# Kernel tuning notes

Hardware: AMD Instinct MI355X
Metric: run time of the kernel (lower is better)

The kernel has to match this reference:

```python
import jax, jax.numpy as jnp
import numpy as np
import math

Q_DIM = 1024
K_DIM = 1024
ATT_DIM = 1024
POS_DIM = 64
B, NQ, NK = 4, 2048, 2048
EPS = 1e-5


def _ln(x, g, b):
    m = jnp.mean(x, axis=-1, keepdims=True)
    v = jnp.var(x, axis=-1, keepdims=True)
    return (x - m) * jax.lax.rsqrt(v + EPS) * g + b


def _sinpos(n, dim):
    # SinPos: exp = 2*arange(dim//2)/dim; pos = p * 10000**-exp; cat(pos, pos+pi/2); sin
    e = 2.0 * jnp.arange(dim // 2, dtype=jnp.float32) / dim      # [dim/2]
    p = jnp.arange(n, dtype=jnp.float32)[:, None]                # [n,1]
    ph = p * jnp.power(10000.0, -e)[None, :]                     # [n,dim/2]
    return jnp.sin(jnp.concatenate([ph, ph + math.pi / 2], axis=1))  # [n,dim]


def setup_inputs() -> dict:
    key = jax.random.key(0)
    ks = jax.random.split(key, 8)
    s = 0.02
    return {
        "q": jax.random.normal(ks[0], (B, NQ, Q_DIM), jnp.float32),
        "k": jax.random.normal(ks[1], (B, NK, K_DIM), jnp.float32),
        "Wq": jax.random.normal(ks[2], (Q_DIM, ATT_DIM), jnp.float32) * s,
        "bq": jnp.zeros((ATT_DIM,), jnp.float32),
        "Wk": jax.random.normal(ks[3], (K_DIM, ATT_DIM), jnp.float32) * s,
        "bk": jnp.zeros((ATT_DIM,), jnp.float32),
        "Wv": jax.random.normal(ks[4], (K_DIM, ATT_DIM), jnp.float32) * s,
        "bv": jnp.zeros((ATT_DIM,), jnp.float32),
        "gq": jnp.ones((ATT_DIM,), jnp.float32), "betaq": jnp.zeros((ATT_DIM,), jnp.float32),
        "gk": jnp.ones((ATT_DIM,), jnp.float32), "betak": jnp.zeros((ATT_DIM,), jnp.float32),
        "gv": jnp.ones((ATT_DIM,), jnp.float32), "betav": jnp.zeros((ATT_DIM,), jnp.float32),
        "Wp": jax.random.normal(ks[5], (POS_DIM, POS_DIM), jnp.float32) * s,
        "bp": jnp.zeros((POS_DIM,), jnp.float32),
    }


def reference(q, k, Wq, bq, Wk, bk, Wv, bv, gq, betaq, gk, betak, gv, betav, Wp, bp):
    qn = _ln(q @ Wq + bq, gq, betaq)          # [B,NQ,D]
    vn = _ln(k @ Wv + bv, gv, betav)          # [B,NK,D]
    kn = _ln(k @ Wk + bk, gk, betak)          # [B,NK,D]
    pos = _sinpos(NK, POS_DIM)                # [NK,P]

    # attention 1: Q=qn, K=kn, V=pos
    s1 = jnp.einsum('bnd,bjd->bnj', qn, kn) * (1.0 / math.sqrt(ATT_DIM))
    a1 = jax.nn.softmax(s1, axis=-1)          # [B,NQ,NK]
    x = jnp.einsum('bnj,jp->bnp', a1, pos)    # [B,NQ,P]

    # pos_net (Linear)
    x = x @ Wp + bp                           # [B,NQ,P]

    # attention 2: Q=x, K=pos, V=vn
    s2 = jnp.einsum('bnp,jp->bnj', x, pos) * (1.0 / math.sqrt(POS_DIM))
    a2 = jax.nn.softmax(s2, axis=-1)          # [B,NQ,NK]
    out = jnp.einsum('bnj,bjd->bnd', a2, vn)  # [B,NQ,D]

    att = jnp.stack([a1, a2], axis=1)         # [B,2,NQ,NK] == torch.cat over head dim
    return out, att
```

## Files before the change

### kernel.cpp

```cpp
#include <hip/hip_runtime.h>
#include <math.h>
#include <stdint.h>


typedef _Float16 f16;
typedef _Float16 f16x4 __attribute__((ext_vector_type(4)));
typedef _Float16 f16x8 __attribute__((ext_vector_type(8)));
typedef float f32x4 __attribute__((ext_vector_type(4)));

static constexpr int CB  = 4;
static constexpr int CNQ = 2048;
static constexpr int CNK = 2048;
static constexpr int CD  = 1024;
static constexpr int CP  = 64;

static __device__ __forceinline__ void async16(const f16* gp, f16* lp) {
  __builtin_amdgcn_global_load_lds(
      (const __attribute__((address_space(1))) void*)(uintptr_t)gp,
      (__attribute__((address_space(3))) void*)(uint32_t)(uintptr_t)lp,
      16, 0, 0);
}

__global__ __launch_bounds__(256) void pos_kernel(f16* __restrict__ posb,
                                                  f16* __restrict__ posTb) {
  int tid = blockIdx.x * 256 + threadIdx.x;
  int p = tid >> 11;
  int j = tid & (CNK - 1);
  int i = p & 31;
  float ph = (float)j * powf(10000.0f, -(float)i * (1.0f / 32.0f));
  float v = (p < 32) ? sinf(ph) : cosf(ph);
  posb[j * CP + p]   = (f16)v;
  posTb[p * CNK + j] = (f16)v;
}

__global__ __launch_bounds__(256) void cvt2_kernel(const float* __restrict__ a,
                                                   const float* __restrict__ b,
                                                   f16* __restrict__ oa,
                                                   f16* __restrict__ ob) {
  const int NF4 = CB * CNQ * CD / 4;
  int tid = blockIdx.x * 256 + threadIdx.x;
  const float* src = (tid < NF4) ? a : b;
  f16* dst = (tid < NF4) ? oa : ob;
  int i = (tid < NF4) ? tid : tid - NF4;
  float4 v = reinterpret_cast<const float4*>(src)[i];
  f16x4 o = {(f16)v.x, (f16)v.y, (f16)v.z, (f16)v.w};
  reinterpret_cast<f16x4*>(dst)[i] = o;
}

__global__ __launch_bounds__(256) void cvtWT_kernel(
    const float* __restrict__ Wq, const float* __restrict__ Wk,
    const float* __restrict__ Wv, f16* __restrict__ WqT, f16* __restrict__ WkvT) {
  __shared__ float t[64][65];
  const float* W = (blockIdx.z == 0) ? Wq : (blockIdx.z == 1) ? Wk : Wv;
  f16* WT = (blockIdx.z == 0) ? WqT : (blockIdx.z == 1) ? WkvT : WkvT + 1024 * 1024;
  int k0 = blockIdx.x * 64, n0 = blockIdx.y * 64;
  int tx = threadIdx.x & 63, ty = threadIdx.x >> 6;
#pragma unroll
  for (int i = 0; i < 16; i++)
    t[ty + 4 * i][tx] = W[(size_t)(k0 + ty + 4 * i) * CD + n0 + tx];
  __syncthreads();
#pragma unroll
  for (int i = 0; i < 16; i++)
    WT[(size_t)(n0 + 4 * i + ty) * CD + k0 + tx] = (f16)t[tx][ty + 4 * i];
}

__global__ __launch_bounds__(256) void transpose_kernel(const f16* __restrict__ in,
                                                        f16* __restrict__ out,
                                                        int ldi) {
  __shared__ f16 t[64][65];
  int n0 = blockIdx.x * 64, d0 = blockIdx.y * 64;
  size_t ibase = (size_t)blockIdx.z * CNK * ldi;
  size_t obase = (size_t)blockIdx.z * CNK * CD;
  int tx = threadIdx.x & 63, ty = threadIdx.x >> 6;
#pragma unroll
  for (int i = 0; i < 16; i++)
    t[ty + 4 * i][tx] = in[ibase + (size_t)(n0 + ty + 4 * i) * ldi + d0 + tx];
  __syncthreads();
#pragma unroll
  for (int i = 0; i < 16; i++)
    out[obase + (size_t)(d0 + ty + 4 * i) * CNK + n0 + tx] = t[tx][ty + 4 * i];
}

template <int BM, int BN>
__device__ __forceinline__ void gemm_core(
    const f16* __restrict__ Ab, const f16* __restrict__ Bb,
    int lda, int ldb, int K, int m0, int n0, f16* sm,
    f32x4 (&acc)[BM / 32][BN / 64]) {
  constexpr int FM = BM / 32, FN = BN / 64;
  constexpr int TI = (BM + BN) / 64;
  constexpr int bufsz = (BM + BN) * 64;
  const int tid = threadIdx.x;
  const int lane = tid & 63, wid = tid >> 6;
  const int wr = wid >> 2, wc = wid & 3;
  const int lrow = lane & 15, kg = lane >> 4;

  auto stage = [&](int i, int kt, int buf) {
    const int s = i * 512 + tid;
    const int row = s >> 3;
    const int cb = (s & 7) << 4;
    const int scb = cb ^ ((row & 7) << 4);
    const f16* src = (i < BM / 64)
        ? Ab + (size_t)(m0 + row) * lda + kt * 64 + (scb >> 1)
        : Bb + (size_t)(n0 + row - BM) * ldb + kt * 64 + (scb >> 1);
    async16(src, &sm[buf * bufsz + s * 8]);
  };

  const int NT = K >> 6;
#pragma unroll
  for (int i = 0; i < TI; i++) stage(i, 0, 0);

  for (int t = 0; t < NT; ++t) {
    const int cur = t & 1;
    if (t + 1 < NT) {
#pragma unroll
      for (int i = 0; i < TI; i++) stage(i, t + 1, cur ^ 1);
      if constexpr (TI == 8) asm volatile("s_waitcnt vmcnt(8)" ::: "memory");
      else                   asm volatile("s_waitcnt vmcnt(6)" ::: "memory");
    } else {
      asm volatile("s_waitcnt vmcnt(0)" ::: "memory");
    }
    __builtin_amdgcn_s_barrier();

    const f16* smA = sm + cur * bufsz;
    const f16* smB = smA + BM * 64;
#pragma unroll
    for (int kk = 0; kk < 2; ++kk) {
      const int Cb = kk * 64 + kg * 16;
      f16x8 af[FM], bf[FN];
#pragma unroll
      for (int m = 0; m < FM; ++m) {
        const int ar = wr * (BM / 2) + m * 16 + lrow;
        af[m] = *reinterpret_cast<const f16x8*>(
            &smA[ar * 64 + ((Cb ^ ((ar & 7) << 4)) >> 1)]);
      }
#pragma unroll
      for (int n = 0; n < FN; ++n) {
        const int br = wc * (BN / 4) + n * 16 + lrow;
        bf[n] = *reinterpret_cast<const f16x8*>(
            &smB[br * 64 + ((Cb ^ ((br & 7) << 4)) >> 1)]);
      }
      __builtin_amdgcn_s_barrier();
      __builtin_amdgcn_s_setprio(1);
#pragma unroll
      for (int m = 0; m < FM; ++m)
#pragma unroll
        for (int n = 0; n < FN; ++n)
          acc[m][n] = __builtin_amdgcn_mfma_f32_16x16x32_f16(af[m], bf[n], acc[m][n], 0, 0, 0);
      __builtin_amdgcn_s_setprio(0);
      __builtin_amdgcn_s_barrier();
    }
  }
}

template <int BM, int BN>
__device__ __forceinline__ void epi_f16(
    f32x4 (&acc)[BM / 32][BN / 64], f16* sm, f16* Cp, int ldc, int m0, int n0) {
  const int tid = threadIdx.x, lane = tid & 63, wid = tid >> 6;
  const int wr = wid >> 2, wc = wid & 3;
  const int rbase = wr * (BM / 2) + (lane >> 4) * 4;
  const int cbase = wc * (BN / 4) + (lane & 15);
  __syncthreads();
#pragma unroll
  for (int mg = 0; mg < BM / 32; mg++)
#pragma unroll
    for (int n = 0; n < BN / 64; n++)
#pragma unroll
      for (int r = 0; r < 4; r++)
        sm[(rbase + mg * 16 + r) * BN + cbase + n * 16] = (f16)acc[mg][n][r];
  __syncthreads();
  constexpr int CH = BM * BN / (512 * 8);
#pragma unroll
  for (int c = 0; c < CH; c++) {
    const int idx = c * 512 + tid;
    const int row = idx / (BN / 8);
    const int cole = (idx % (BN / 8)) * 8;
    f16x8 v = *reinterpret_cast<const f16x8*>(&sm[row * BN + cole]);
    *reinterpret_cast<f16x8*>(Cp + (size_t)(m0 + row) * ldc + n0 + cole) = v;
  }
}

template <int BM, int BN>
__device__ __forceinline__ void epi_exp(
    f32x4 (&acc)[BM / 32][BN / 64], f16* sm, float* psum, f16* Cp, int ldc,
    int m0, int n0, float scale, float* PSrow) {
  const int tid = threadIdx.x, lane = tid & 63, wid = tid >> 6;
  const int wr = wid >> 2, wc = wid & 3;
  const int rbase = wr * (BM / 2) + (lane >> 4) * 4;
  const int cbase = wc * (BN / 4) + (lane & 15);
  __syncthreads();
  if (tid < BM) psum[tid] = 0.f;
#pragma unroll
  for (int mg = 0; mg < BM / 32; mg++)
#pragma unroll
    for (int n = 0; n < BN / 64; n++)
#pragma unroll
      for (int r = 0; r < 4; r++)
        sm[(rbase + mg * 16 + r) * BN + cbase + n * 16] =
            (f16)__expf(acc[mg][n][r] * scale);
  __syncthreads();
  constexpr int CH = BM * BN / (512 * 8);
#pragma unroll
  for (int c = 0; c < CH; c++) {
    const int idx = c * 512 + tid;
    const int row = idx / (BN / 8);
    const int cole = (idx % (BN / 8)) * 8;
    f16x8 v = *reinterpret_cast<const f16x8*>(&sm[row * BN + cole]);
    *reinterpret_cast<f16x8*>(Cp + (size_t)(m0 + row) * ldc + n0 + cole) = v;
    float p = 0.f;
#pragma unroll
    for (int j = 0; j < 8; j++) p += (float)v[j];
#pragma unroll
    for (int o = 1; o < 32; o <<= 1) p += __shfl_xor(p, o);
    if ((lane & 31) == 0) atomicAdd(&psum[row], p);
  }
  __syncthreads();
  if (tid < BM) PSrow[tid] = psum[tid];
}

template <int BM, int BN>
__device__ __forceinline__ void epi_f32(
    f32x4 (&acc)[BM / 32][BN / 64], f16* smh, float* Cp, int ldc, int m0, int n0) {
  float* st = (float*)smh;
  const int tid = threadIdx.x, lane = tid & 63, wid = tid >> 6;
  const int wr = wid >> 2, wc = wid & 3;
  const int cbase = wc * (BN / 4) + (lane & 15);
#pragma unroll
  for (int half = 0; half < 2; half++) {
    __syncthreads();
    if (wr == half) {
#pragma unroll
      for (int mg = 0; mg < BM / 32; mg++)
#pragma unroll
        for (int r = 0; r < 4; r++) {
          const int rloc = (lane >> 4) * 4 + mg * 16 + r;
#pragma unroll
          for (int n = 0; n < BN / 64; n++)
            st[rloc * BN + cbase + n * 16] = acc[mg][n][r];
        }
    }
    __syncthreads();
    constexpr int CH = (BM / 2) * BN / (512 * 4);
#pragma unroll
    for (int c = 0; c < CH; c++) {
      const int idx = c * 512 + tid;
      const int row = idx / (BN / 4);
      const int cole = (idx % (BN / 4)) * 4;
      float4 v = *reinterpret_cast<const float4*>(&st[row * BN + cole]);
      *reinterpret_cast<float4*>(
          Cp + (size_t)(m0 + half * (BM / 2) + row) * ldc + n0 + cole) = v;
    }
  }
}

__global__ __launch_bounds__(512) void gemmIn_kernel(
    const f16* __restrict__ q16, const f16* __restrict__ WqT, f16* __restrict__ tmpq,
    const f16* __restrict__ k16, const f16* __restrict__ WkvT, f16* __restrict__ tmp2) {
  __shared__ __attribute__((aligned(16))) f16 sm[2][(256 + 128) * 64];
  const int b = blockIdx.x;
  const int swz = (b & 7) * 96 + (b >> 3);
  const f16 *A, *B;
  f16* C;
  int ldc, m0, n0;
  if (swz < 256) {
    const int by = swz >> 5, bx = swz & 31;
    A = q16; B = WqT; C = tmpq; ldc = 1024; m0 = bx * 256; n0 = by * 128;
  } else {
    const int idx = swz - 256;
    const int by = idx >> 5, bx = idx & 31;
    A = k16; B = WkvT; C = tmp2; ldc = 2048; m0 = bx * 256; n0 = by * 128;
  }
  f32x4 acc[8][2] = {};
  gemm_core<256, 128>(A, B, 1024, 1024, 1024, m0, n0, &sm[0][0], acc);
  epi_f16<256, 128>(acc, &sm[0][0], C, ldc, m0, n0);
}

__global__ __launch_bounds__(512) void gemmS1_kernel(
    const f16* __restrict__ qn, const f16* __restrict__ kn,
    f16* __restrict__ e1, float* __restrict__ PS) {
  __shared__ __attribute__((aligned(16))) f16 sm[2][(256 + 256) * 64];
  __shared__ float psum[256];
  const int b = blockIdx.x;
  const int swz = (b & 7) * 32 + (b >> 3);
  const int bz = swz >> 6;
  const int rem = swz & 63;
  const int by = rem >> 3, bx = rem & 7;
  const int m0 = bx * 256, n0 = by * 256;
  const f16* Ab = qn + (size_t)bz * 2048 * 1024;
  const f16* Bb = kn + (size_t)bz * 2048 * 2048;
  f16* Cp = e1 + (size_t)bz * 2048 * 2048;
  f32x4 acc[8][4] = {};
  gemm_core<256, 256>(Ab, Bb, 1024, 2048, 1024, m0, n0, &sm[0][0], acc);
  epi_exp<256, 256>(acc, &sm[0][0], psum, Cp, 2048, m0, n0, 0.03125f,
                    PS + (size_t)by * 8192 + bz * 2048 + m0);
}

__global__ __launch_bounds__(512) void gemmOut_kernel(
    const f16* __restrict__ e2, const f16* __restrict__ vnT, float* __restrict__ out) {
  __shared__ __attribute__((aligned(16))) f16 sm[2][(256 + 128) * 64];
  const int b = blockIdx.x;
  const int swz = (b & 7) * 32 + (b >> 3);
  const int bz = swz >> 6;
  const int rem = swz & 63;
  const int by = rem >> 3, bx = rem & 7;
  const int m0 = bx * 256, n0 = by * 128;
  const f16* Ab = e2 + (size_t)bz * 2048 * 2048;
  const f16* Bb = vnT + (size_t)bz * 1024 * 2048;
  float* Cp = out + (size_t)bz * 2048 * 1024;
  f32x4 acc[8][2] = {};
  gemm_core<256, 128>(Ab, Bb, 2048, 2048, 2048, m0, n0, &sm[0][0], acc);
  epi_f32<256, 128>(acc, &sm[0][0], Cp, 1024, m0, n0);
}

__global__ __launch_bounds__(256) void ln3_kernel(
    f16* __restrict__ tmpq, f16* __restrict__ tmp2,
    const float* __restrict__ bq, const float* __restrict__ gq, const float* __restrict__ beq,
    const float* __restrict__ bk, const float* __restrict__ gk, const float* __restrict__ bek,
    const float* __restrict__ bv, const float* __restrict__ gv, const float* __restrict__ bev) {
  __shared__ float rs_[4], rq_[4];
  const int z = blockIdx.y;
  f16* rp;
  const float *bias, *g, *beta;
  if (z == 0)      { rp = tmpq + (size_t)blockIdx.x * 1024;        bias = bq; g = gq; beta = beq; }
  else if (z == 1) { rp = tmp2 + (size_t)blockIdx.x * 2048;        bias = bk; g = gk; beta = bek; }
  else             { rp = tmp2 + (size_t)blockIdx.x * 2048 + 1024; bias = bv; g = gv; beta = bev; }
  const int t = threadIdx.x;
  f16x4 v = *reinterpret_cast<const f16x4*>(rp + t * 4);
  float y[4], s = 0.f, q = 0.f;
#pragma unroll
  for (int j = 0; j < 4; j++) {
    y[j] = (float)v[j] + bias[t * 4 + j];
    s += y[j]; q += y[j] * y[j];
  }
#pragma unroll
  for (int o = 32; o; o >>= 1) { s += __shfl_xor(s, o); q += __shfl_xor(q, o); }
  if ((t & 63) == 0) { rs_[t >> 6] = s; rq_[t >> 6] = q; }
  __syncthreads();
  s = rs_[0] + rs_[1] + rs_[2] + rs_[3];
  q = rq_[0] + rq_[1] + rq_[2] + rq_[3];
  const float mean = s * (1.0f / CD);
  const float rstd = rsqrtf(q * (1.0f / CD) - mean * mean + 1e-5f);
  f16x4 o;
#pragma unroll
  for (int j = 0; j < 4; j++) {
    int c = t * 4 + j;
    o[j] = (f16)((y[j] - mean) * rstd * g[c] + beta[c]);
  }
  *reinterpret_cast<f16x4*>(rp + t * 4) = o;
}

__global__ __launch_bounds__(256) void norm1_kernel(
    const f16* __restrict__ e1, const float* __restrict__ PS,
    float* __restrict__ inv1, float* __restrict__ att) {
  const int row = blockIdx.x;
  const int b = row >> 11, n = row & (CNQ - 1);
  float s = 0.f;
#pragma unroll
  for (int j = 0; j < 8; j++) s += PS[j * (CB * CNQ) + row];
  const float iv = 1.0f / s;
  if (threadIdx.x == 0) inv1[row] = iv;
  const int t = threadIdx.x;
  float* rp = att + ((size_t)(b << 1) * CNQ + n) * CNK;
  f16x8 v = *reinterpret_cast<const f16x8*>(e1 + (size_t)row * CNK + t * 8);
  float4 w0 = {(float)v[0] * iv, (float)v[1] * iv, (float)v[2] * iv, (float)v[3] * iv};
  float4 w1 = {(float)v[4] * iv, (float)v[5] * iv, (float)v[6] * iv, (float)v[7] * iv};
  reinterpret_cast<float4*>(rp)[t * 2]     = w0;
  reinterpret_cast<float4*>(rp)[t * 2 + 1] = w1;
}

__global__ __launch_bounds__(256) void xgemm_kernel(
    const f16* __restrict__ e1, const f16* __restrict__ posTb, float* __restrict__ xw) {
  constexpr int BM = 64, BN = 64;
  __shared__ __attribute__((aligned(16))) f16 As[BM * 32];
  __shared__ __attribute__((aligned(16))) f16 Bs[BN * 32];
  const int lane = threadIdx.x & 63;
  const int wave = threadIdx.x >> 6;
  const int wr = wave >> 1, wc = wave & 1;
  const int m0 = blockIdx.x * BM;
  const int kbase = blockIdx.z * 1024;
  const int srow = lane >> 2;
  const int scol = (lane & 3) * 8;
  const int lrow = lane & 15;
  const int kg = lane >> 4;
  f32x4 acc[2][2] = {};
  for (int k0 = 0; k0 < 1024; k0 += 32) {
    __syncthreads();
#pragma unroll
    for (int i = wave; i < 8; i += 4) {
      if (i < 4)
        async16(e1 + (size_t)(m0 + i * 16 + srow) * CNK + kbase + k0 + scol, &As[i * 512]);
      else
        async16(posTb + (size_t)((i - 4) * 16 + srow) * CNK + kbase + k0 + scol,
                &Bs[(i - 4) * 512]);
    }
    __syncthreads();
    f16x8 af[2], bfr[2];
#pragma unroll
    for (int m = 0; m < 2; m++)
      af[m] = *reinterpret_cast<const f16x8*>(&As[(wr * 32 + m * 16 + lrow) * 32 + kg * 8]);
#pragma unroll
    for (int n = 0; n < 2; n++)
      bfr[n] = *reinterpret_cast<const f16x8*>(&Bs[(wc * 32 + n * 16 + lrow) * 32 + kg * 8]);
#pragma unroll
    for (int m = 0; m < 2; m++)
#pragma unroll
      for (int n = 0; n < 2; n++)
        acc[m][n] = __builtin_amdgcn_mfma_f32_16x16x32_f16(af[m], bfr[n], acc[m][n], 0, 0, 0);
  }
  float* Cp = xw + (size_t)blockIdx.z * (CB * CNQ) * CP;
  const int crow = m0 + wr * 32 + (lane >> 4) * 4;
  const int ccol = wc * 32 + (lane & 15);
#pragma unroll
  for (int m = 0; m < 2; m++)
#pragma unroll
    for (int n = 0; n < 2; n++)
#pragma unroll
      for (int r = 0; r < 4; r++)
        Cp[(size_t)(crow + m * 16 + r) * CP + ccol + n * 16] = acc[m][n][r];
}

__global__ __launch_bounds__(128) void attn2_kernel(
    const float* __restrict__ xw, const float* __restrict__ Wp,
    const float* __restrict__ bp, const f16* __restrict__ posb,
    const float* __restrict__ inv1, f16* __restrict__ e2,
    float* __restrict__ att) {
  __shared__ __attribute__((aligned(16))) f16 shm[32 * 2048 + 32 * 64];
  __shared__ float rsum[32];
  f16* e2lds = shm;
  f16* xpb = shm + 32 * 2048;
  float* xs = (float*)shm;
  float* Wps = (float*)shm + 32 * 64;
  const int tid = threadIdx.x, l = tid & 63, w = tid >> 6;
  const int r0 = blockIdx.x * 32;
#pragma unroll
  for (int i = 0; i < 16; i++) {
    const int row = w * 16 + i;
    const size_t gi = (size_t)(r0 + row) * CP + l;
    xs[row * 64 + l] = (xw[gi] + xw[(size_t)(CB * CNQ) * CP + gi]) * inv1[r0 + row];
  }
#pragma unroll
  for (int i = w; i < 64; i += 2) Wps[i * 64 + l] = Wp[i * 64 + l];
  const float bpl = bp[l];
  __syncthreads();
  const int rb = w * 16;
#pragma unroll 2
  for (int i = 0; i < 16; i++) {
    float a = bpl;
#pragma unroll 8
    for (int p = 0; p < 64; p++) a = fmaf(xs[(rb + i) * 64 + p], Wps[p * 64 + l], a);
    xpb[(rb + i) * 64 + l] = (f16)a;
  }
  __syncthreads();
  const f16x8 af0 = *reinterpret_cast<const f16x8*>(&xpb[(rb + (l & 15)) * 64 + (l >> 4) * 8]);
  const f16x8 af1 = *reinterpret_cast<const f16x8*>(&xpb[(rb + (l & 15)) * 64 + 32 + (l >> 4) * 8]);
  float rs[4] = {0.f, 0.f, 0.f, 0.f};
  for (int jt = 0; jt < CNK / 64; jt++) {
#pragma unroll
    for (int q4 = 0; q4 < 4; q4++) {
      const int j = jt * 64 + q4 * 16 + (l & 15);
      const f16* pp = posb + (size_t)j * CP + (l >> 4) * 8;
      f16x8 b0 = *reinterpret_cast<const f16x8*>(pp);
      f16x8 b1 = *reinterpret_cast<const f16x8*>(pp + 32);
      f32x4 c = {};
      c = __builtin_amdgcn_mfma_f32_16x16x32_f16(af0, b0, c, 0, 0, 0);
      c = __builtin_amdgcn_mfma_f32_16x16x32_f16(af1, b1, c, 0, 0, 0);
#pragma unroll
      for (int r = 0; r < 4; r++) {
        float ev = __expf(c[r] * 0.125f);
        rs[r] += ev;
        e2lds[(rb + (l >> 4) * 4 + r) * 2048 + j] = (f16)ev;
      }
    }
  }
#pragma unroll
  for (int r = 0; r < 4; r++) {
#pragma unroll
    for (int o = 1; o < 16; o <<= 1) rs[r] += __shfl_xor(rs[r], o);
    if ((l & 15) == 0) rsum[rb + (l >> 4) * 4 + r] = rs[r];
  }
  __syncthreads();
  const int b = r0 >> 11, nloc = r0 & (CNQ - 1);
  float* attb = att + ((size_t)((b << 1) + 1) * CNQ + nloc) * CNK;
  f16* e2b = e2 + (size_t)r0 * CNK;
  for (int row = 0; row < 32; row++) {
    const float iv = 1.0f / rsum[row];
    const f16x8 a0 = *reinterpret_cast<const f16x8*>(&e2lds[row * 2048 + tid * 16]);
    const f16x8 a1 = *reinterpret_cast<const f16x8*>(&e2lds[row * 2048 + tid * 16 + 8]);
    float4 w0 = {(float)a0[0] * iv, (float)a0[1] * iv, (float)a0[2] * iv, (float)a0[3] * iv};
    float4 w1 = {(float)a0[4] * iv, (float)a0[5] * iv, (float)a0[6] * iv, (float)a0[7] * iv};
    float4 w2 = {(float)a1[0] * iv, (float)a1[1] * iv, (float)a1[2] * iv, (float)a1[3] * iv};
    float4 w3 = {(float)a1[4] * iv, (float)a1[5] * iv, (float)a1[6] * iv, (float)a1[7] * iv};
    float* ap = attb + (size_t)row * CNK + tid * 16;
    reinterpret_cast<float4*>(ap)[0] = w0;
    reinterpret_cast<float4*>(ap)[1] = w1;
    reinterpret_cast<float4*>(ap)[2] = w2;
    reinterpret_cast<float4*>(ap)[3] = w3;
    f16x8 h0 = {(f16)w0.x, (f16)w0.y, (f16)w0.z, (f16)w0.w,
                (f16)w1.x, (f16)w1.y, (f16)w1.z, (f16)w1.w};
    f16x8 h1 = {(f16)w2.x, (f16)w2.y, (f16)w2.z, (f16)w2.w,
                (f16)w3.x, (f16)w3.y, (f16)w3.z, (f16)w3.w};
    f16* ep = e2b + (size_t)row * CNK + tid * 16;
    *reinterpret_cast<f16x8*>(ep)     = h0;
    *reinterpret_cast<f16x8*>(ep + 8) = h1;
  }
}

extern "C" void kernel_launch(void* const* d_in, const int* in_sizes, int n_in,
                              void* d_out, int out_size, void* d_ws, size_t ws_size,
                              hipStream_t stream) {
  (void)in_sizes; (void)n_in; (void)out_size; (void)ws_size;
  const float* q    = (const float*)d_in[0];
  const float* k    = (const float*)d_in[1];
  const float* Wq   = (const float*)d_in[2];
  const float* bq   = (const float*)d_in[3];
  const float* Wk   = (const float*)d_in[4];
  const float* bk   = (const float*)d_in[5];
  const float* Wv   = (const float*)d_in[6];
  const float* bv   = (const float*)d_in[7];
  const float* gq   = (const float*)d_in[8];
  const float* betaq= (const float*)d_in[9];
  const float* gk   = (const float*)d_in[10];
  const float* betak= (const float*)d_in[11];
  const float* gv   = (const float*)d_in[12];
  const float* betav= (const float*)d_in[13];
  const float* Wp   = (const float*)d_in[14];
  const float* bp   = (const float*)d_in[15];

  float* out = (float*)d_out;
  float* att = out + (size_t)CB * CNQ * CD;
  char* ws = (char*)d_ws;
  const size_t MB = 1ull << 20;

  f16* q16   = (f16*)(ws);
  f16* k16   = (f16*)(ws + 16 * MB);
  f16* e1    = (f16*)(ws);
  f16* e2    = (f16*)(ws);
  f16* WqT   = (f16*)(ws + 32 * MB);
  f16* WkvT  = (f16*)(ws + 34 * MB);
  f16* posb  = (f16*)(ws + 38 * MB);
  f16* posTb = (f16*)(ws + 38 * MB + 256 * 1024);
  float* xw  = (float*)(ws + 38 * MB + 512 * 1024);
  float* PS  = (float*)(ws + 42 * MB + 512 * 1024);
  float* inv1= (float*)(ws + 42 * MB + 768 * 1024);
  f16* tmpq  = (f16*)(ws + 43 * MB);
  f16* tmp2  = (f16*)(ws + 59 * MB);
  f16* vnT   = (f16*)(ws + 91 * MB);
  f16* qn = tmpq;
  f16* kn = tmp2;
  f16* vn = tmp2 + 1024;

  pos_kernel<<<(CP * CNK) / 256, 256, 0, stream>>>(posb, posTb);
  cvt2_kernel<<<2 * (CB * CNQ * CD / 4) / 256, 256, 0, stream>>>(q, k, q16, k16);
  cvtWT_kernel<<<dim3(16, 16, 3), 256, 0, stream>>>(Wq, Wk, Wv, WqT, WkvT);

  gemmIn_kernel<<<768, 512, 0, stream>>>(q16, WqT, tmpq, k16, WkvT, tmp2);
  ln3_kernel<<<dim3(CB * CNQ, 3), 256, 0, stream>>>(
      tmpq, tmp2, bq, gq, betaq, bk, gk, betak, bv, gv, betav);
  transpose_kernel<<<dim3(CNK / 64, CD / 64, CB), 256, 0, stream>>>(vn, vnT, 2048);

  gemmS1_kernel<<<256, 512, 0, stream>>>(qn, kn, e1, PS);
  norm1_kernel<<<CB * CNQ, 256, 0, stream>>>(e1, PS, inv1, att);

  xgemm_kernel<<<dim3(CB * CNQ / 64, 1, 2), 256, 0, stream>>>(e1, posTb, xw);
  attn2_kernel<<<CB * CNQ / 32, 128, 0, stream>>>(xw, Wp, bp, posb, inv1, e2, att);

  gemmOut_kernel<<<256, 512, 0, stream>>>(e2, vnT, out);
}
```

Baseline: 324.1 us.

## Fuse prep kernels, triple-buffer GEMM core, fold softmax normalization into xgemm

Merges the pos, conversion and weight-transpose kernels into one prep launch. Switches the shared GEMM mainloop to a three-stage LDS pipeline. Shrinks the gemmS1 tile to 256x128 with 512 blocks and writes row partial sums directly instead of through LDS atomics. Removes norm1_kernel by having xgemm write the normalized attention-1 probabilities while it streams e1 tiles, and attn2 recomputes the inverse sums from PS. The aim is fewer launches, one less full pass over e1, and better latency hiding, at the cost of more LDS per block (possibly lower occupancy) and 16-way partial-sum reductions.

```diff
diff --git a/kernel.cpp b/kernel.cpp
--- a/kernel.cpp
+++ b/kernel.cpp
@@ -21,47 +21,49 @@
       16, 0, 0);
 }
 
-__global__ __launch_bounds__(256) void pos_kernel(f16* __restrict__ posb,
-                                                  f16* __restrict__ posTb) {
-  int tid = blockIdx.x * 256 + threadIdx.x;
-  int p = tid >> 11;
-  int j = tid & (CNK - 1);
-  int i = p & 31;
-  float ph = (float)j * powf(10000.0f, -(float)i * (1.0f / 32.0f));
-  float v = (p < 32) ? sinf(ph) : cosf(ph);
-  posb[j * CP + p]   = (f16)v;
-  posTb[p * CNK + j] = (f16)v;
-}
-
-__global__ __launch_bounds__(256) void cvt2_kernel(const float* __restrict__ a,
-                                                   const float* __restrict__ b,
-                                                   f16* __restrict__ oa,
-                                                   f16* __restrict__ ob) {
-  const int NF4 = CB * CNQ * CD / 4;
-  int tid = blockIdx.x * 256 + threadIdx.x;
-  const float* src = (tid < NF4) ? a : b;
-  f16* dst = (tid < NF4) ? oa : ob;
-  int i = (tid < NF4) ? tid : tid - NF4;
-  float4 v = reinterpret_cast<const float4*>(src)[i];
-  f16x4 o = {(f16)v.x, (f16)v.y, (f16)v.z, (f16)v.w};
-  reinterpret_cast<f16x4*>(dst)[i] = o;
-}
-
-__global__ __launch_bounds__(256) void cvtWT_kernel(
+__global__ __launch_bounds__(256) void prep_kernel(
+    const float* __restrict__ q, const float* __restrict__ k,
     const float* __restrict__ Wq, const float* __restrict__ Wk,
-    const float* __restrict__ Wv, f16* __restrict__ WqT, f16* __restrict__ WkvT) {
-  __shared__ float t[64][65];
-  const float* W = (blockIdx.z == 0) ? Wq : (blockIdx.z == 1) ? Wk : Wv;
-  f16* WT = (blockIdx.z == 0) ? WqT : (blockIdx.z == 1) ? WkvT : WkvT + 1024 * 1024;
-  int k0 = blockIdx.x * 64, n0 = blockIdx.y * 64;
-  int tx = threadIdx.x & 63, ty = threadIdx.x >> 6;
-#pragma unroll
-  for (int i = 0; i < 16; i++)
-    t[ty + 4 * i][tx] = W[(size_t)(k0 + ty + 4 * i) * CD + n0 + tx];
-  __syncthreads();
-#pragma unroll
-  for (int i = 0; i < 16; i++)
-    WT[(size_t)(n0 + 4 * i + ty) * CD + k0 + tx] = (f16)t[tx][ty + 4 * i];
+    const float* __restrict__ Wv,
+    f16* __restrict__ q16, f16* __restrict__ k16,
+    f16* __restrict__ WqT, f16* __restrict__ WkvT,
+    f16* __restrict__ posb, f16* __restrict__ posTb) {
+  const int b = blockIdx.x;
+  if (b < 512) {
+    int tid = b * 256 + threadIdx.x;
+    int p = tid >> 11;
+    int j = tid & (CNK - 1);
+    int i = p & 31;
+    float ph = (float)j * powf(10000.0f, -(float)i * (1.0f / 32.0f));
+    float v = (p < 32) ? sinf(ph) : cosf(ph);
+    posb[j * CP + p]   = (f16)v;
+    posTb[p * CNK + j] = (f16)v;
+  } else if (b < 512 + 16384) {
+    const int NF4 = CB * CNQ * CD / 4;
+    int tid = (b - 512) * 256 + threadIdx.x;
+    const float* src = (tid < NF4) ? q : k;
+    f16* dst = (tid < NF4) ? q16 : k16;
+    int i = (tid < NF4) ? tid : tid - NF4;
+    float4 v = reinterpret_cast<const float4*>(src)[i];
+    f16x4 o = {(f16)v.x, (f16)v.y, (f16)v.z, (f16)v.w};
+    reinterpret_cast<f16x4*>(dst)[i] = o;
+  } else {
+    __shared__ float t[64][65];
+    const int idx = b - 16896;
+    const int z = idx >> 8;
+    const int rem = idx & 255;
+    const float* W = (z == 0) ? Wq : (z == 1) ? Wk : Wv;
+    f16* WT = (z == 0) ? WqT : (z == 1) ? WkvT : WkvT + 1024 * 1024;
+    int k0 = (rem & 15) * 64, n0 = (rem >> 4) * 64;
+    int tx = threadIdx.x & 63, ty = threadIdx.x >> 6;
+#pragma unroll
+    for (int i = 0; i < 16; i++)
+      t[ty + 4 * i][tx] = W[(size_t)(k0 + ty + 4 * i) * CD + n0 + tx];
+    __syncthreads();
+#pragma unroll
+    for (int i = 0; i < 16; i++)
+      WT[(size_t)(n0 + 4 * i + ty) * CD + k0 + tx] = (f16)t[tx][ty + 4 * i];
+  }
 }
 
 __global__ __launch_bounds__(256) void transpose_kernel(const f16* __restrict__ in,
@@ -82,7 +84,7 @@
 }
 
 template <int BM, int BN>
-__device__ __forceinline__ void gemm_core(
+__device__ __forceinline__ void gemm_core3(
     const f16* __restrict__ Ab, const f16* __restrict__ Bb,
     int lda, int ldb, int K, int m0, int n0, f16* sm,
     f32x4 (&acc)[BM / 32][BN / 64]) {
@@ -108,20 +110,23 @@
   const int NT = K >> 6;
 #pragma unroll
   for (int i = 0; i < TI; i++) stage(i, 0, 0);
+#pragma unroll
+  for (int i = 0; i < TI; i++) stage(i, 1, 1);
 
   for (int t = 0; t < NT; ++t) {
-    const int cur = t & 1;
-    if (t + 1 < NT) {
-#pragma unroll
-      for (int i = 0; i < TI; i++) stage(i, t + 1, cur ^ 1);
-      if constexpr (TI == 8) asm volatile("s_waitcnt vmcnt(8)" ::: "memory");
-      else                   asm volatile("s_waitcnt vmcnt(6)" ::: "memory");
+    if (t + 2 < NT) {
+      const int b2 = (t + 2) % 3;
+#pragma unroll
+      for (int i = 0; i < TI; i++) stage(i, t + 2, b2);
+      asm volatile("s_waitcnt vmcnt(12)" ::: "memory");
+    } else if (t + 2 == NT) {
+      asm volatile("s_waitcnt vmcnt(6)" ::: "memory");
     } else {
       asm volatile("s_waitcnt vmcnt(0)" ::: "memory");
     }
     __builtin_amdgcn_s_barrier();
 
-    const f16* smA = sm + cur * bufsz;
+    const f16* smA = sm + (t % 3) * bufsz;
     const f16* smB = smA + BM * 64;
 #pragma unroll
     for (int kk = 0; kk < 2; ++kk) {
@@ -183,12 +188,12 @@
 __device__ __forceinline__ void epi_exp(
     f32x4 (&acc)[BM / 32][BN / 64], f16* sm, float* psum, f16* Cp, int ldc,
     int m0, int n0, float scale, float* PSrow) {
+  constexpr int SL = BN / 8;
   const int tid = threadIdx.x, lane = tid & 63, wid = tid >> 6;
   const int wr = wid >> 2, wc = wid & 3;
   const int rbase = wr * (BM / 2) + (lane >> 4) * 4;
   const int cbase = wc * (BN / 4) + (lane & 15);
   __syncthreads();
-  if (tid < BM) psum[tid] = 0.f;
 #pragma unroll
   for (int mg = 0; mg < BM / 32; mg++)
 #pragma unroll
@@ -202,16 +207,16 @@
 #pragma unroll
   for (int c = 0; c < CH; c++) {
     const int idx = c * 512 + tid;
-    const int row = idx / (BN / 8);
-    const int cole = (idx % (BN / 8)) * 8;
+    const int row = idx / SL;
+    const int cole = (idx % SL) * 8;
     f16x8 v = *reinterpret_cast<const f16x8*>(&sm[row * BN + cole]);
     *reinterpret_cast<f16x8*>(Cp + (size_t)(m0 + row) * ldc + n0 + cole) = v;
     float p = 0.f;
 #pragma unroll
     for (int j = 0; j < 8; j++) p += (float)v[j];
 #pragma unroll
-    for (int o = 1; o < 32; o <<= 1) p += __shfl_xor(p, o);
-    if ((lane & 31) == 0) atomicAdd(&psum[row], p);
+    for (int o = 1; o < SL; o <<= 1) p += __shfl_xor(p, o);
+    if ((lane & (SL - 1)) == 0) psum[row] = p;
   }
   __syncthreads();
   if (tid < BM) PSrow[tid] = psum[tid];
@@ -255,7 +260,7 @@
 __global__ __launch_bounds__(512) void gemmIn_kernel(
     const f16* __restrict__ q16, const f16* __restrict__ WqT, f16* __restrict__ tmpq,
     const f16* __restrict__ k16, const f16* __restrict__ WkvT, f16* __restrict__ tmp2) {
-  __shared__ __attribute__((aligned(16))) f16 sm[2][(256 + 128) * 64];
+  __shared__ __attribute__((aligned(16))) f16 sm[3 * (256 + 128) * 64];
   const int b = blockIdx.x;
   const int swz = (b & 7) * 96 + (b >> 3);
   const f16 *A, *B;
@@ -270,33 +275,33 @@
     A = k16; B = WkvT; C = tmp2; ldc = 2048; m0 = bx * 256; n0 = by * 128;
   }
   f32x4 acc[8][2] = {};
-  gemm_core<256, 128>(A, B, 1024, 1024, 1024, m0, n0, &sm[0][0], acc);
-  epi_f16<256, 128>(acc, &sm[0][0], C, ldc, m0, n0);
+  gemm_core3<256, 128>(A, B, 1024, 1024, 1024, m0, n0, sm, acc);
+  epi_f16<256, 128>(acc, sm, C, ldc, m0, n0);
 }
 
 __global__ __launch_bounds__(512) void gemmS1_kernel(
     const f16* __restrict__ qn, const f16* __restrict__ kn,
     f16* __restrict__ e1, float* __restrict__ PS) {
-  __shared__ __attribute__((aligned(16))) f16 sm[2][(256 + 256) * 64];
+  __shared__ __attribute__((aligned(16))) f16 sm[3 * (256 + 128) * 64];
   __shared__ float psum[256];
   const int b = blockIdx.x;
-  const int swz = (b & 7) * 32 + (b >> 3);
-  const int bz = swz >> 6;
-  const int rem = swz & 63;
+  const int swz = (b & 7) * 64 + (b >> 3);
+  const int bz = swz >> 7;
+  const int rem = swz & 127;
   const int by = rem >> 3, bx = rem & 7;
-  const int m0 = bx * 256, n0 = by * 256;
+  const int m0 = bx * 256, n0 = by * 128;
   const f16* Ab = qn + (size_t)bz * 2048 * 1024;
   const f16* Bb = kn + (size_t)bz * 2048 * 2048;
   f16* Cp = e1 + (size_t)bz * 2048 * 2048;
-  f32x4 acc[8][4] = {};
-  gemm_core<256, 256>(Ab, Bb, 1024, 2048, 1024, m0, n0, &sm[0][0], acc);
-  epi_exp<256, 256>(acc, &sm[0][0], psum, Cp, 2048, m0, n0, 0.03125f,
+  f32x4 acc[8][2] = {};
+  gemm_core3<256, 128>(Ab, Bb, 1024, 2048, 1024, m0, n0, sm, acc);
+  epi_exp<256, 128>(acc, sm, psum, Cp, 2048, m0, n0, 0.03125f,
                     PS + (size_t)by * 8192 + bz * 2048 + m0);
 }
 
 __global__ __launch_bounds__(512) void gemmOut_kernel(
     const f16* __restrict__ e2, const f16* __restrict__ vnT, float* __restrict__ out) {
-  __shared__ __attribute__((aligned(16))) f16 sm[2][(256 + 128) * 64];
+  __shared__ __attribute__((aligned(16))) f16 sm[3 * (256 + 128) * 64];
   const int b = blockIdx.x;
   const int swz = (b & 7) * 32 + (b >> 3);
   const int bz = swz >> 6;
@@ -307,8 +312,8 @@
   const f16* Bb = vnT + (size_t)bz * 1024 * 2048;
   float* Cp = out + (size_t)bz * 2048 * 1024;
   f32x4 acc[8][2] = {};
-  gemm_core<256, 128>(Ab, Bb, 2048, 2048, 2048, m0, n0, &sm[0][0], acc);
-  epi_f32<256, 128>(acc, &sm[0][0], Cp, 1024, m0, n0);
+  gemm_core3<256, 128>(Ab, Bb, 2048, 2048, 2048, m0, n0, sm, acc);
+  epi_f32<256, 128>(acc, sm, Cp, 1024, m0, n0);
 }
 
 __global__ __launch_bounds__(256) void ln3_kernel(
@@ -348,32 +353,16 @@
   *reinterpret_cast<f16x4*>(rp + t * 4) = o;
 }
 
-__global__ __launch_bounds__(256) void norm1_kernel(
-    const f16* __restrict__ e1, const float* __restrict__ PS,
-    float* __restrict__ inv1, float* __restrict__ att) {
-  const int row = blockIdx.x;
-  const int b = row >> 11, n = row & (CNQ - 1);
-  float s = 0.f;
-#pragma unroll
-  for (int j = 0; j < 8; j++) s += PS[j * (CB * CNQ) + row];
-  const float iv = 1.0f / s;
-  if (threadIdx.x == 0) inv1[row] = iv;
-  const int t = threadIdx.x;
-  float* rp = att + ((size_t)(b << 1) * CNQ + n) * CNK;
-  f16x8 v = *reinterpret_cast<const f16x8*>(e1 + (size_t)row * CNK + t * 8);
-  float4 w0 = {(float)v[0] * iv, (float)v[1] * iv, (float)v[2] * iv, (float)v[3] * iv};
-  float4 w1 = {(float)v[4] * iv, (float)v[5] * iv, (float)v[6] * iv, (float)v[7] * iv};
-  reinterpret_cast<float4*>(rp)[t * 2]     = w0;
-  reinterpret_cast<float4*>(rp)[t * 2 + 1] = w1;
-}
-
 __global__ __launch_bounds__(256) void xgemm_kernel(
-    const f16* __restrict__ e1, const f16* __restrict__ posTb, float* __restrict__ xw) {
+    const f16* __restrict__ e1, const f16* __restrict__ posTb,
+    const float* __restrict__ PS, float* __restrict__ xw, float* __restrict__ att) {
   constexpr int BM = 64, BN = 64;
   __shared__ __attribute__((aligned(16))) f16 As[BM * 32];
   __shared__ __attribute__((aligned(16))) f16 Bs[BN * 32];
-  const int lane = threadIdx.x & 63;
-  const int wave = threadIdx.x >> 6;
+  __shared__ float invs[BM];
+  const int tid = threadIdx.x;
+  const int lane = tid & 63;
+  const int wave = tid >> 6;
   const int wr = wave >> 1, wc = wave & 1;
   const int m0 = blockIdx.x * BM;
   const int kbase = blockIdx.z * 1024;
@@ -381,6 +370,18 @@
   const int scol = (lane & 3) * 8;
   const int lrow = lane & 15;
   const int kg = lane >> 4;
+
+  if (tid < BM) {
+    float s = 0.f;
+#pragma unroll
+    for (int j = 0; j < 16; j++) s += PS[j * (CB * CNQ) + m0 + tid];
+    invs[tid] = 1.0f / s;
+  }
+
+  const int bb = m0 >> 11, nloc = m0 & (CNQ - 1);
+  float* attb = att + ((size_t)(bb << 1) * CNQ + nloc) * CNK + kbase;
+  const int arow = tid >> 2, acol = (tid & 3) * 8;
+
   f32x4 acc[2][2] = {};
   for (int k0 = 0; k0 < 1024; k0 += 32) {
     __syncthreads();
@@ -405,6 +406,15 @@
 #pragma unroll
       for (int n = 0; n < 2; n++)
         acc[m][n] = __builtin_amdgcn_mfma_f32_16x16x32_f16(af[m], bfr[n], acc[m][n], 0, 0, 0);
+    {
+      const float iv = invs[arow];
+      f16x8 v = *reinterpret_cast<const f16x8*>(&As[arow * 32 + acol]);
+      float4 w0 = {(float)v[0] * iv, (float)v[1] * iv, (float)v[2] * iv, (float)v[3] * iv};
+      float4 w1 = {(float)v[4] * iv, (float)v[5] * iv, (float)v[6] * iv, (float)v[7] * iv};
+      float* ap = attb + (size_t)arow * CNK + k0 + acol;
+      reinterpret_cast<float4*>(ap)[0] = w0;
+      reinterpret_cast<float4*>(ap)[1] = w1;
+    }
   }
   float* Cp = xw + (size_t)blockIdx.z * (CB * CNQ) * CP;
   const int crow = m0 + wr * 32 + (lane >> 4) * 4;
@@ -421,21 +431,29 @@
 __global__ __launch_bounds__(128) void attn2_kernel(
     const float* __restrict__ xw, const float* __restrict__ Wp,
     const float* __restrict__ bp, const f16* __restrict__ posb,
-    const float* __restrict__ inv1, f16* __restrict__ e2,
+    const float* __restrict__ PS, f16* __restrict__ e2,
     float* __restrict__ att) {
   __shared__ __attribute__((aligned(16))) f16 shm[32 * 2048 + 32 * 64];
   __shared__ float rsum[32];
+  __shared__ float invs[32];
   f16* e2lds = shm;
   f16* xpb = shm + 32 * 2048;
   float* xs = (float*)shm;
   float* Wps = (float*)shm + 32 * 64;
   const int tid = threadIdx.x, l = tid & 63, w = tid >> 6;
   const int r0 = blockIdx.x * 32;
+  if (tid < 32) {
+    float s = 0.f;
+#pragma unroll
+    for (int j = 0; j < 16; j++) s += PS[j * (CB * CNQ) + r0 + tid];
+    invs[tid] = 1.0f / s;
+  }
+  __syncthreads();
 #pragma unroll
   for (int i = 0; i < 16; i++) {
     const int row = w * 16 + i;
     const size_t gi = (size_t)(r0 + row) * CP + l;
-    xs[row * 64 + l] = (xw[gi] + xw[(size_t)(CB * CNQ) * CP + gi]) * inv1[r0 + row];
+    xs[row * 64 + l] = (xw[gi] + xw[(size_t)(CB * CNQ) * CP + gi]) * invs[row];
   }
 #pragma unroll
   for (int i = w; i < 64; i += 2) Wps[i * 64 + l] = Wp[i * 64 + l];
@@ -540,7 +558,6 @@
   f16* posTb = (f16*)(ws + 38 * MB + 256 * 1024);
   float* xw  = (float*)(ws + 38 * MB + 512 * 1024);
   float* PS  = (float*)(ws + 42 * MB + 512 * 1024);
-  float* inv1= (float*)(ws + 42 * MB + 768 * 1024);
   f16* tmpq  = (f16*)(ws + 43 * MB);
   f16* tmp2  = (f16*)(ws + 59 * MB);
   f16* vnT   = (f16*)(ws + 91 * MB);
@@ -548,20 +565,18 @@
   f16* kn = tmp2;
   f16* vn = tmp2 + 1024;
 
-  pos_kernel<<<(CP * CNK) / 256, 256, 0, stream>>>(posb, posTb);
-  cvt2_kernel<<<2 * (CB * CNQ * CD / 4) / 256, 256, 0, stream>>>(q, k, q16, k16);
-  cvtWT_kernel<<<dim3(16, 16, 3), 256, 0, stream>>>(Wq, Wk, Wv, WqT, WkvT);
+  prep_kernel<<<512 + 16384 + 768, 256, 0, stream>>>(
+      q, k, Wq, Wk, Wv, q16, k16, WqT, WkvT, posb, posTb);
 
   gemmIn_kernel<<<768, 512, 0, stream>>>(q16, WqT, tmpq, k16, WkvT, tmp2);
   ln3_kernel<<<dim3(CB * CNQ, 3), 256, 0, stream>>>(
       tmpq, tmp2, bq, gq, betaq, bk, gk, betak, bv, gv, betav);
   transpose_kernel<<<dim3(CNK / 64, CD / 64, CB), 256, 0, stream>>>(vn, vnT, 2048);
 
-  gemmS1_kernel<<<256, 512, 0, stream>>>(qn, kn, e1, PS);
-  norm1_kernel<<<CB * CNQ, 256, 0, stream>>>(e1, PS, inv1, att);
-
-  xgemm_kernel<<<dim3(CB * CNQ / 64, 1, 2), 256, 0, stream>>>(e1, posTb, xw);
-  attn2_kernel<<<CB * CNQ / 32, 128, 0, stream>>>(xw, Wp, bp, posb, inv1, e2, att);
+  gemmS1_kernel<<<512, 512, 0, stream>>>(qn, kn, e1, PS);
+
+  xgemm_kernel<<<dim3(CB * CNQ / 64, 1, 2), 256, 0, stream>>>(e1, posTb, PS, xw, att);
+  attn2_kernel<<<CB * CNQ / 32, 128, 0, stream>>>(xw, Wp, bp, posb, PS, e2, att);
 
   gemmOut_kernel<<<256, 512, 0, stream>>>(e2, vnT, out);
 }
```

Measured after the change: 323.7 us. No clear change (-0.1%).
